# Kernel optimization log

Measured on AMD Instinct MI355X. Metric: run time of the kernel, lower is better.

The kernel has to match this reference:

```python
import jax, jax.numpy as jnp
from jax import lax
import numpy as np

B, C, H, W, T = 8, 256, 31, 31, 7  # batch, channels, search HxW, template size


def setup_inputs() -> dict:
    key = jax.random.key(0)
    k1, k2, k3, k4 = jax.random.split(key, 4)
    sr = jax.random.normal(k1, (B, C, H, W), jnp.float32)
    tmpl = jax.random.normal(k2, (B, C, T, T), jnp.float32)
    # offset/mask conv params (module zero-inits; use small random as a trained stand-in)
    w_om = jax.random.normal(k3, (3 * T * T, C, 3, 3), jnp.float32) * 0.01
    b_om = jax.random.normal(k4, (3 * T * T,), jnp.float32) * 0.01
    return {"sr_features": sr, "template_features": tmpl,
            "w_offset_mask": w_om, "b_offset_mask": b_om}


def _modulated_deform_xcorr(sr, tmpl, w_om, b_om):
    Bs, Cs, Hs, Ws = sr.shape
    Ts = tmpl.shape[-1]
    K = Ts * Ts
    # 3x3 'same' conv predicting per-pixel offsets (y, x) and modulation mask
    om = lax.conv_general_dilated(sr, w_om, (1, 1), 'SAME',
                                  dimension_numbers=('NCHW', 'OIHW', 'NCHW'))
    om = om + b_om[None, :, None, None]
    off_y, off_x, mask = om[:, :K], om[:, K:2 * K], om[:, 2 * K:]
    mask = jax.nn.sigmoid(mask)
    oh, ow = Hs - Ts + 1, Ws - Ts + 1  # stride 1, padding 0, dilation 1
    off_y = off_y[:, :, :oh, :ow]
    off_x = off_x[:, :, :oh, :ow]
    mask = mask[:, :, :oh, :ow]
    # kernel-tap base offsets (k = p*T + q)
    ky = jnp.repeat(jnp.arange(Ts), Ts).astype(sr.dtype)  # (K,)
    kx = jnp.tile(jnp.arange(Ts), Ts).astype(sr.dtype)    # (K,)
    iy = jnp.arange(oh, dtype=sr.dtype)
    ix = jnp.arange(ow, dtype=sr.dtype)
    ys = iy[None, None, :, None] + ky[None, :, None, None] + off_y  # (B,K,oh,ow)
    xs = ix[None, None, None, :] + kx[None, :, None, None] + off_x  # (B,K,oh,ow)
    y0 = jnp.floor(ys)
    x0 = jnp.floor(xs)
    wy = ys - y0
    wx = xs - x0
    bidx = jnp.arange(Bs)[:, None, None, None]

    def gather(yf, xf):
        # zero-padded gather at integer corner (yf, xf); returns (B,K,oh,ow,C)
        valid = (yf >= 0) & (yf <= Hs - 1) & (xf >= 0) & (xf <= Ws - 1)
        yc = jnp.clip(yf, 0, Hs - 1).astype(jnp.int32)
        xc = jnp.clip(xf, 0, Ws - 1).astype(jnp.int32)
        v = sr[bidx, :, yc, xc]  # (B,K,oh,ow,C)
        return v * valid[..., None].astype(sr.dtype)

    one = jnp.asarray(1, sr.dtype)
    v = (((one - wy) * (one - wx))[..., None] * gather(y0, x0)
         + ((one - wy) * wx)[..., None] * gather(y0, x0 + 1)
         + (wy * (one - wx))[..., None] * gather(y0 + 1, x0)
         + (wy * wx)[..., None] * gather(y0 + 1, x0 + 1))
    # depthwise xcorr: template acts as per-(batch,channel) kernel, modulated by mask
    tmpl_k = tmpl.reshape(Bs, Cs, K)
    out = jnp.einsum('bck,bkij,bkijc->bcij', tmpl_k, mask, v)  # (B,C,oh,ow)
    return out


def reference(sr_features, template_features, w_offset_mask, b_offset_mask):
    return _modulated_deform_xcorr(sr_features, template_features,
                                   w_offset_mask, b_offset_mask)
```

## Files before the change

kernel.cpp:

```cpp
#include <hip/hip_runtime.h>
#include <hip/hip_bf16.h>
#include <math.h>

#define B_ 8
#define C_ 256
#define H_ 31
#define W_ 31
#define T_ 7
#define K_ 49
#define OC_ 147
#define OCP 160
#define OH_ 25
#define OW_ 25
#define NSP 961
#define OSP 625
#define KK_ 2304

typedef __bf16 bf16x8 __attribute__((ext_vector_type(8)));
typedef float f32x4 __attribute__((ext_vector_type(4)));

#define OFFB_SRT 0
#define OFFB_TMT 3936256
#define OFFB_WPK 4136960
#define OFFB_BIAS 4874240
#define OFFB_OM  4874880

__device__ inline float blo(unsigned u) { return __uint_as_float(u << 16); }
__device__ inline float bhi(unsigned u) { return __uint_as_float(u & 0xffff0000u); }

__global__ __launch_bounds__(256) void k1_transpose_sr(const float* __restrict__ sr,
                                                       __hip_bfloat16* __restrict__ srT) {
    __shared__ float tile[32][33];
    int bx = blockIdx.x;
    int b = bx / 248;
    int rem = bx % 248;
    int ct = rem / 31;
    int st = rem % 31;
    int c0 = ct * 32, s0 = st * 32;
    int tx = threadIdx.x, ty = threadIdx.y;
    #pragma unroll
    for (int rr = 0; rr < 4; rr++) {
        int c = c0 + ty + rr * 8;
        int s = s0 + tx;
        if (s < NSP) tile[ty + rr * 8][tx] = sr[(b * C_ + c) * NSP + s];
    }
    __syncthreads();
    #pragma unroll
    for (int rr = 0; rr < 4; rr++) {
        int s = s0 + ty + rr * 8;
        int c = c0 + tx;
        if (s < NSP) srT[((long)b * NSP + s) * C_ + c] = __float2bfloat16(tile[tx][ty + rr * 8]);
    }
}

__global__ __launch_bounds__(256) void k2_transpose_tmpl(const float* __restrict__ tm,
                                                         __hip_bfloat16* __restrict__ tmT) {
    int bx = blockIdx.x;
    int b = bx / K_;
    int k = bx % K_;
    int c = threadIdx.x;
    tmT[(b * K_ + k) * C_ + c] = __float2bfloat16(tm[(b * C_ + c) * K_ + k]);
}

__global__ __launch_bounds__(256) void k2b_pack_w(const float* __restrict__ w,
                                                  const float* __restrict__ bias,
                                                  __hip_bfloat16* __restrict__ wPk,
                                                  float* __restrict__ biasP) {
    if (blockIdx.x == 0 && threadIdx.x < OCP)
        biasP[threadIdx.x] = (threadIdx.x < OC_) ? bias[threadIdx.x] : 0.f;
    int i = blockIdx.x * 256 + threadIdx.x;
    if (i >= 46080) return;
    int l = i & 63;
    int fid = i >> 6;
    int mf = fid % 5;
    int mh = (fid / 5) % 2;
    int ks = (fid / 10) % 2;
    int s  = (fid / 20) % 9;
    int cg = fid / 180;
    int oc = mh * 80 + mf * 16 + (l & 15);
    int cbase = cg * 64 + ks * 32 + (l >> 4) * 8;
    bf16x8 v;
    #pragma unroll
    for (int jj = 0; jj < 8; jj++) {
        float f = (oc < OC_) ? w[oc * KK_ + (cbase + jj) * 9 + s] : 0.f;
        v[jj] = (__bf16)f;
    }
    *reinterpret_cast<bf16x8*>(wPk + ((long)i << 3)) = v;
}

__global__ __launch_bounds__(128) void k3_mfma(const __hip_bfloat16* __restrict__ srT,
                                               const __hip_bfloat16* __restrict__ wPk,
                                               float* __restrict__ om) {
    __shared__ __hip_bfloat16 lds[88 * 72];
    int sb = (blockIdx.x & 7) * 100 + (blockIdx.x >> 3);
    int b = sb / 100;
    int rem = sb % 100;
    int i = rem / 4;
    int cg = rem % 4;
    int tid = threadIdx.x;

    const __hip_bfloat16* srTb = srT + (long)b * NSP * C_ + cg * 64;
    for (int o = tid; o < 648; o += 128) {
        int ryx = o >> 3;
        int c8 = (o & 7) * 8;
        int yy = ryx / 27;
        int xi = ryx - yy * 27;
        int y = i - 1 + yy;
        int x = xi - 1;
        bf16x8 v = {};
        if (y >= 0 && x >= 0)
            v = *reinterpret_cast<const bf16x8*>(srTb + (y * W_ + x) * C_ + c8);
        *reinterpret_cast<bf16x8*>(&lds[ryx * 72 + c8]) = v;
    }
    __syncthreads();

    int wv = tid >> 6;
    int l = tid & 63;
    int lr = l & 15, lg = l >> 4;

    f32x4 acc[5][2] = {};
    const bf16x8* apk = reinterpret_cast<const bf16x8*>(wPk);

    #pragma unroll
    for (int dy = 0; dy < 3; ++dy) {
        #pragma unroll
        for (int dx = 0; dx < 3; ++dx) {
            int s = dy * 3 + dx;
            #pragma unroll
            for (int ks = 0; ks < 2; ++ks) {
                int e0 = (dy * 27 + dx + lr) * 72 + ks * 32 + lg * 8;
                bf16x8 b0 = *reinterpret_cast<const bf16x8*>(&lds[e0]);
                bf16x8 b1 = *reinterpret_cast<const bf16x8*>(&lds[e0 + 16 * 72]);
                const bf16x8* ap = apk + (long)((((cg * 9 + s) * 2 + ks) * 2 + wv) * 5) * 64 + l;
                #pragma unroll
                for (int mf = 0; mf < 5; ++mf) {
                    bf16x8 a = ap[mf * 64];
                    acc[mf][0] = __builtin_amdgcn_mfma_f32_16x16x32_bf16(a, b0, acc[mf][0], 0, 0, 0);
                    acc[mf][1] = __builtin_amdgcn_mfma_f32_16x16x32_bf16(a, b1, acc[mf][1], 0, 0, 0);
                }
            }
        }
    }

    #pragma unroll
    for (int nf = 0; nf < 2; ++nf) {
        int j = nf * 16 + lr;
        if (j < OW_) {
            float* ob = om + (long)((b * OH_ + i) * 4 + cg) * (OW_ * OCP) + j * OCP + wv * 80 + lg * 4;
            #pragma unroll
            for (int mf = 0; mf < 5; ++mf)
                *reinterpret_cast<f32x4*>(ob + mf * 16) = acc[mf][nf];
        }
    }
}

__global__ __launch_bounds__(128) void k4_gather(const __hip_bfloat16* __restrict__ srT,
                                                 const __hip_bfloat16* __restrict__ tmT,
                                                 const float* __restrict__ om,
                                                 const float* __restrict__ biasP,
                                                 float* __restrict__ out) {
    __shared__ float lom[OCP];
    __shared__ int4 loff[K_];
    __shared__ float4 lwt[K_];
    int sb = (blockIdx.x & 7) * 625 + (blockIdx.x >> 3);
    int b = sb / OSP;
    int rem = sb % OSP;
    int i = rem / OW_;
    int j = rem % OW_;
    int t = threadIdx.x;

    if (t < 40) {
        f32x4 s = *reinterpret_cast<const f32x4*>(biasP + t * 4);
        const float* ob = om + (long)(b * OH_ + i) * (4 * OW_ * OCP) + j * OCP + t * 4;
        #pragma unroll
        for (int cg = 0; cg < 4; cg++)
            s += *reinterpret_cast<const f32x4*>(ob + cg * (OW_ * OCP));
        *reinterpret_cast<f32x4*>(lom + t * 4) = s;
    }
    __syncthreads();

    if (t < K_) {
        float oy = lom[t];
        float ox = lom[K_ + t];
        float mk = 1.f / (1.f + expf(-lom[2 * K_ + t]));
        float ys = (float)(i + t / T_) + oy;
        float xs = (float)(j + t % T_) + ox;
        float y0f = floorf(ys);
        float x0f = floorf(xs);
        float wy = ys - y0f, wx = xs - x0f;
        bool vy0 = (y0f >= 0.f) && (y0f <= 30.f);
        bool vy1 = (y0f >= -1.f) && (y0f <= 29.f);
        bool vx0 = (x0f >= 0.f) && (x0f <= 30.f);
        bool vx1 = (x0f >= -1.f) && (x0f <= 29.f);
        int iy = (int)y0f;
        int ix = (int)x0f;
        int cy0 = min(max(iy, 0), 30), cy1 = min(max(iy + 1, 0), 30);
        int cx0 = min(max(ix, 0), 30), cx1 = min(max(ix + 1, 0), 30);
        float a00 = (1.f - wy) * (1.f - wx), a01 = (1.f - wy) * wx;
        float a10 = wy * (1.f - wx), a11 = wy * wx;
        lwt[t] = make_float4(mk * a00 * (float)(vy0 && vx0),
                             mk * a01 * (float)(vy0 && vx1),
                             mk * a10 * (float)(vy1 && vx0),
                             mk * a11 * (float)(vy1 && vx1));
        loff[t] = make_int4((cy0 * W_ + cx0) * 128, (cy0 * W_ + cx1) * 128,
                            (cy1 * W_ + cx0) * 128, (cy1 * W_ + cx1) * 128);
    }
    __syncthreads();

    const unsigned* srU = reinterpret_cast<const unsigned*>(srT) + (long)b * NSP * 128;
    const unsigned* tmU = reinterpret_cast<const unsigned*>(tmT) + (long)b * K_ * 128;
    float acc0 = 0.f, acc1 = 0.f;
    for (int k = 0; k < K_; ++k) {
        int4 o = loff[k];
        float4 wv = lwt[k];
        unsigned u00 = srU[o.x + t];
        unsigned u01 = srU[o.y + t];
        unsigned u10 = srU[o.z + t];
        unsigned u11 = srU[o.w + t];
        unsigned tu = tmU[(k << 7) + t];
        float s0 = wv.x * blo(u00);
        s0 = fmaf(wv.y, blo(u01), s0);
        s0 = fmaf(wv.z, blo(u10), s0);
        s0 = fmaf(wv.w, blo(u11), s0);
        float s1 = wv.x * bhi(u00);
        s1 = fmaf(wv.y, bhi(u01), s1);
        s1 = fmaf(wv.z, bhi(u10), s1);
        s1 = fmaf(wv.w, bhi(u11), s1);
        acc0 = fmaf(blo(tu), s0, acc0);
        acc1 = fmaf(bhi(tu), s1, acc1);
    }
    long ob = ((long)(b * C_ + 2 * t) * OH_ + i) * OW_ + j;
    out[ob] = acc0;
    out[ob + (long)OH_ * OW_] = acc1;
}

extern "C" void kernel_launch(void* const* d_in, const int* in_sizes, int n_in,
                              void* d_out, int out_size, void* d_ws, size_t ws_size,
                              hipStream_t stream) {
    const float* sr = (const float*)d_in[0];
    const float* tm = (const float*)d_in[1];
    const float* w  = (const float*)d_in[2];
    const float* bs = (const float*)d_in[3];
    float* out = (float*)d_out;
    char* wsb = (char*)d_ws;
    __hip_bfloat16* srT = (__hip_bfloat16*)(wsb + OFFB_SRT);
    __hip_bfloat16* tmT = (__hip_bfloat16*)(wsb + OFFB_TMT);
    __hip_bfloat16* wPk = (__hip_bfloat16*)(wsb + OFFB_WPK);
    float* biasP = (float*)(wsb + OFFB_BIAS);
    float* om = (float*)(wsb + OFFB_OM);

    k1_transpose_sr<<<8 * 8 * 31, dim3(32, 8), 0, stream>>>(sr, srT);
    k2_transpose_tmpl<<<B_ * K_, 256, 0, stream>>>(tm, tmT);
    k2b_pack_w<<<180, 256, 0, stream>>>(w, bs, wPk, biasP);
    k3_mfma<<<B_ * OH_ * 4, 128, 0, stream>>>(srT, wPk, om);
    k4_gather<<<B_ * OSP, 128, 0, stream>>>(srT, tmT, om, biasP, out);
}
```

Baseline: 134.7 us.

## Merge prep kernels into one launch and split gather taps across waves

The three preprocessing kernels (sr transpose, template transpose, weight pack) become one kernel that dispatches on block index, which removes two launches and their serialization gaps. The gather kernel now has each lane load 8-byte chunks holding 4 channels. The 49 taps are split between the block's two wavefronts, and the partial sums are combined through shared memory. This gives wider loads and more loads in flight per lane, in exchange for an extra barrier and a shared-memory reduction.

After: 141.6 us. +5.1%, slower.

```diff
diff --git a/kernel.cpp b/kernel.cpp
--- a/kernel.cpp
+++ b/kernel.cpp
@@ -28,64 +28,66 @@
 __device__ inline float blo(unsigned u) { return __uint_as_float(u << 16); }
 __device__ inline float bhi(unsigned u) { return __uint_as_float(u & 0xffff0000u); }
 
-__global__ __launch_bounds__(256) void k1_transpose_sr(const float* __restrict__ sr,
-                                                       __hip_bfloat16* __restrict__ srT) {
+__global__ __launch_bounds__(256) void prep(const float* __restrict__ sr,
+                                            const float* __restrict__ tm,
+                                            const float* __restrict__ w,
+                                            const float* __restrict__ bias,
+                                            __hip_bfloat16* __restrict__ srT,
+                                            __hip_bfloat16* __restrict__ tmT,
+                                            __hip_bfloat16* __restrict__ wPk,
+                                            float* __restrict__ biasP) {
     __shared__ float tile[32][33];
-    int bx = blockIdx.x;
-    int b = bx / 248;
-    int rem = bx % 248;
-    int ct = rem / 31;
-    int st = rem % 31;
-    int c0 = ct * 32, s0 = st * 32;
-    int tx = threadIdx.x, ty = threadIdx.y;
-    #pragma unroll
-    for (int rr = 0; rr < 4; rr++) {
-        int c = c0 + ty + rr * 8;
-        int s = s0 + tx;
-        if (s < NSP) tile[ty + rr * 8][tx] = sr[(b * C_ + c) * NSP + s];
-    }
-    __syncthreads();
-    #pragma unroll
-    for (int rr = 0; rr < 4; rr++) {
-        int s = s0 + ty + rr * 8;
-        int c = c0 + tx;
-        if (s < NSP) srT[((long)b * NSP + s) * C_ + c] = __float2bfloat16(tile[tx][ty + rr * 8]);
-    }
-}
-
-__global__ __launch_bounds__(256) void k2_transpose_tmpl(const float* __restrict__ tm,
-                                                         __hip_bfloat16* __restrict__ tmT) {
-    int bx = blockIdx.x;
-    int b = bx / K_;
-    int k = bx % K_;
-    int c = threadIdx.x;
-    tmT[(b * K_ + k) * C_ + c] = __float2bfloat16(tm[(b * C_ + c) * K_ + k]);
-}
-
-__global__ __launch_bounds__(256) void k2b_pack_w(const float* __restrict__ w,
-                                                  const float* __restrict__ bias,
-                                                  __hip_bfloat16* __restrict__ wPk,
-                                                  float* __restrict__ biasP) {
-    if (blockIdx.x == 0 && threadIdx.x < OCP)
-        biasP[threadIdx.x] = (threadIdx.x < OC_) ? bias[threadIdx.x] : 0.f;
-    int i = blockIdx.x * 256 + threadIdx.x;
-    if (i >= 46080) return;
-    int l = i & 63;
-    int fid = i >> 6;
-    int mf = fid % 5;
-    int mh = (fid / 5) % 2;
-    int ks = (fid / 10) % 2;
-    int s  = (fid / 20) % 9;
-    int cg = fid / 180;
-    int oc = mh * 80 + mf * 16 + (l & 15);
-    int cbase = cg * 64 + ks * 32 + (l >> 4) * 8;
-    bf16x8 v;
-    #pragma unroll
-    for (int jj = 0; jj < 8; jj++) {
-        float f = (oc < OC_) ? w[oc * KK_ + (cbase + jj) * 9 + s] : 0.f;
-        v[jj] = (__bf16)f;
-    }
-    *reinterpret_cast<bf16x8*>(wPk + ((long)i << 3)) = v;
+    int bid = blockIdx.x;
+    int t = threadIdx.x;
+
+    if (bid < 1984) {
+        int b = bid / 248;
+        int rem = bid % 248;
+        int ct = rem / 31;
+        int st = rem % 31;
+        int c0 = ct * 32, s0 = st * 32;
+        int tx = t & 31, ty = t >> 5;
+        #pragma unroll
+        for (int rr = 0; rr < 4; rr++) {
+            int c = c0 + ty + rr * 8;
+            int s = s0 + tx;
+            if (s < NSP) tile[ty + rr * 8][tx] = sr[(b * C_ + c) * NSP + s];
+        }
+        __syncthreads();
+        #pragma unroll
+        for (int rr = 0; rr < 4; rr++) {
+            int s = s0 + ty + rr * 8;
+            int c = c0 + tx;
+            if (s < NSP) srT[((long)b * NSP + s) * C_ + c] = __float2bfloat16(tile[tx][ty + rr * 8]);
+        }
+    } else if (bid < 2376) {
+        int bx = bid - 1984;
+        int b = bx / K_;
+        int k = bx % K_;
+        tmT[(b * K_ + k) * C_ + t] = __float2bfloat16(tm[(b * C_ + t) * K_ + k]);
+    } else {
+        if (bid == 2376 && t < OCP)
+            biasP[t] = (t < OC_) ? bias[t] : 0.f;
+        int i = (bid - 2376) * 256 + t;
+        if (i < 46080) {
+            int l = i & 63;
+            int fid = i >> 6;
+            int mf = fid % 5;
+            int mh = (fid / 5) % 2;
+            int ks = (fid / 10) % 2;
+            int s  = (fid / 20) % 9;
+            int cg = fid / 180;
+            int oc = mh * 80 + mf * 16 + (l & 15);
+            int cbase = cg * 64 + ks * 32 + (l >> 4) * 8;
+            bf16x8 v;
+            #pragma unroll
+            for (int jj = 0; jj < 8; jj++) {
+                float f = (oc < OC_) ? w[oc * KK_ + (cbase + jj) * 9 + s] : 0.f;
+                v[jj] = (__bf16)f;
+            }
+            *reinterpret_cast<bf16x8*>(wPk + ((long)i << 3)) = v;
+        }
+    }
 }
 
 __global__ __launch_bounds__(128) void k3_mfma(const __hip_bfloat16* __restrict__ srT,
@@ -162,6 +164,7 @@
     __shared__ float lom[OCP];
     __shared__ int4 loff[K_];
     __shared__ float4 lwt[K_];
+    __shared__ float red[64][4];
     int sb = (blockIdx.x & 7) * 625 + (blockIdx.x >> 3);
     int b = sb / OSP;
     int rem = sb % OSP;
@@ -202,36 +205,55 @@
                              mk * a01 * (float)(vy0 && vx1),
                              mk * a10 * (float)(vy1 && vx0),
                              mk * a11 * (float)(vy1 && vx1));
-        loff[t] = make_int4((cy0 * W_ + cx0) * 128, (cy0 * W_ + cx1) * 128,
-                            (cy1 * W_ + cx0) * 128, (cy1 * W_ + cx1) * 128);
-    }
-    __syncthreads();
-
-    const unsigned* srU = reinterpret_cast<const unsigned*>(srT) + (long)b * NSP * 128;
-    const unsigned* tmU = reinterpret_cast<const unsigned*>(tmT) + (long)b * K_ * 128;
-    float acc0 = 0.f, acc1 = 0.f;
-    for (int k = 0; k < K_; ++k) {
+        loff[t] = make_int4((cy0 * W_ + cx0) * 512, (cy0 * W_ + cx1) * 512,
+                            (cy1 * W_ + cx0) * 512, (cy1 * W_ + cx1) * 512);
+    }
+    __syncthreads();
+
+    int wv = t >> 6, lane = t & 63;
+    const char* srBase = (const char*)srT + (long)b * NSP * 512;
+    const char* tmBase = (const char*)tmT + (long)b * K_ * 512;
+    unsigned laneb = lane << 3;
+    float a0 = 0.f, a1 = 0.f, a2 = 0.f, a3 = 0.f;
+    int kb = wv ? 25 : 0, ke = wv ? 49 : 25;
+
+    for (int k = kb; k < ke; ++k) {
         int4 o = loff[k];
-        float4 wv = lwt[k];
-        unsigned u00 = srU[o.x + t];
-        unsigned u01 = srU[o.y + t];
-        unsigned u10 = srU[o.z + t];
-        unsigned u11 = srU[o.w + t];
-        unsigned tu = tmU[(k << 7) + t];
-        float s0 = wv.x * blo(u00);
-        s0 = fmaf(wv.y, blo(u01), s0);
-        s0 = fmaf(wv.z, blo(u10), s0);
-        s0 = fmaf(wv.w, blo(u11), s0);
-        float s1 = wv.x * bhi(u00);
-        s1 = fmaf(wv.y, bhi(u01), s1);
-        s1 = fmaf(wv.z, bhi(u10), s1);
-        s1 = fmaf(wv.w, bhi(u11), s1);
-        acc0 = fmaf(blo(tu), s0, acc0);
-        acc1 = fmaf(bhi(tu), s1, acc1);
-    }
-    long ob = ((long)(b * C_ + 2 * t) * OH_ + i) * OW_ + j;
-    out[ob] = acc0;
-    out[ob + (long)OH_ * OW_] = acc1;
+        float4 wt = lwt[k];
+        uint2 u00 = *reinterpret_cast<const uint2*>(srBase + (unsigned)o.x + laneb);
+        uint2 u01 = *reinterpret_cast<const uint2*>(srBase + (unsigned)o.y + laneb);
+        uint2 u10 = *reinterpret_cast<const uint2*>(srBase + (unsigned)o.z + laneb);
+        uint2 u11 = *reinterpret_cast<const uint2*>(srBase + (unsigned)o.w + laneb);
+        uint2 tu  = *reinterpret_cast<const uint2*>(tmBase + ((unsigned)k << 9) + laneb);
+        float s;
+        s = wt.x * blo(u00.x); s = fmaf(wt.y, blo(u01.x), s);
+        s = fmaf(wt.z, blo(u10.x), s); s = fmaf(wt.w, blo(u11.x), s);
+        a0 = fmaf(blo(tu.x), s, a0);
+        s = wt.x * bhi(u00.x); s = fmaf(wt.y, bhi(u01.x), s);
+        s = fmaf(wt.z, bhi(u10.x), s); s = fmaf(wt.w, bhi(u11.x), s);
+        a1 = fmaf(bhi(tu.x), s, a1);
+        s = wt.x * blo(u00.y); s = fmaf(wt.y, blo(u01.y), s);
+        s = fmaf(wt.z, blo(u10.y), s); s = fmaf(wt.w, blo(u11.y), s);
+        a2 = fmaf(blo(tu.y), s, a2);
+        s = wt.x * bhi(u00.y); s = fmaf(wt.y, bhi(u01.y), s);
+        s = fmaf(wt.z, bhi(u10.y), s); s = fmaf(wt.w, bhi(u11.y), s);
+        a3 = fmaf(bhi(tu.y), s, a3);
+    }
+
+    if (wv) {
+        red[lane][0] = a0; red[lane][1] = a1;
+        red[lane][2] = a2; red[lane][3] = a3;
+    }
+    __syncthreads();
+    if (!wv) {
+        a0 += red[lane][0]; a1 += red[lane][1];
+        a2 += red[lane][2]; a3 += red[lane][3];
+        long ob = ((long)(b * C_ + 4 * lane) * OH_ + i) * OW_ + j;
+        out[ob] = a0;
+        out[ob + OSP] = a1;
+        out[ob + 2 * OSP] = a2;
+        out[ob + 3 * OSP] = a3;
+    }
 }
 
 extern "C" void kernel_launch(void* const* d_in, const int* in_sizes, int n_in,
@@ -249,9 +271,7 @@
     float* biasP = (float*)(wsb + OFFB_BIAS);
     float* om = (float*)(wsb + OFFB_OM);
 
-    k1_transpose_sr<<<8 * 8 * 31, dim3(32, 8), 0, stream>>>(sr, srT);
-    k2_transpose_tmpl<<<B_ * K_, 256, 0, stream>>>(tm, tmT);
-    k2b_pack_w<<<180, 256, 0, stream>>>(w, bs, wPk, biasP);
+    prep<<<2556, 256, 0, stream>>>(sr, tm, w, bs, srT, tmT, wPk, biasP);
     k3_mfma<<<B_ * OH_ * 4, 128, 0, stream>>>(srT, wPk, om);
     k4_gather<<<B_ * OSP, 128, 0, stream>>>(srT, tmT, om, biasP, out);
 }
```
